# Kernel optimization log

Measured on AMD Instinct MI355X. Metric: run time of the kernel, lower is better.

The kernel has to match this reference:

```python
import jax, jax.numpy as jnp
import numpy as np

B, T, C, H = 2, 2048, 1024, 16
D = C // H  # head dim = 64

def setup_inputs() -> dict:
    key = jax.random.key(0)
    ks = jax.random.split(key, 5)
    s = 0.02
    return {
        "x": jax.random.normal(ks[0], (B, T, C), dtype=jnp.float32),
        "Wqkv": jax.random.normal(ks[1], (C, 3 * C), dtype=jnp.float32) * s,
        "bqkv": jnp.zeros((3 * C,), dtype=jnp.float32),
        "Wproj": jax.random.normal(ks[2], (C, C), dtype=jnp.float32) * s,
        "bproj": jnp.zeros((C,), dtype=jnp.float32),
    }

def reference(x, Wqkv, bqkv, Wproj, bproj):
    b, t, c = x.shape
    qkv = x @ Wqkv + bqkv                       # [B,T,3C]
    q, k, v = jnp.split(qkv, 3, axis=-1)
    # [B,T,C] -> [B,H,T,D]
    q = q.reshape(b, t, H, D).transpose(0, 2, 1, 3)
    k = k.reshape(b, t, H, D).transpose(0, 2, 1, 3)
    v = v.reshape(b, t, H, D).transpose(0, 2, 1, 3)
    scale = 1.0 / np.sqrt(D).astype(np.float32)
    attn = jnp.einsum('bhqd,bhkd->bhqk', q, k) * scale  # [B,H,T,T]
    causal = jnp.tril(jnp.ones((t, t), dtype=bool))
    attn = jnp.where(causal, attn, jnp.float32(-jnp.inf))
    attn = jax.nn.softmax(attn, axis=-1)
    y = jnp.einsum('bhqk,bhkd->bhqd', attn, v)          # [B,H,T,D]
    y = y.transpose(0, 2, 1, 3).reshape(b, t, c)        # [B,T,C]
    return y @ Wproj + bproj
```

## Files before the change

kernel.cpp:

```cpp
#include <hip/hip_runtime.h>
#include <stdint.h>

#define B_ 2
#define T_ 2048
#define C_ 1024
#define H_ 16
#define D_ 64
#define M_ (B_*T_)
#define BHTD_ (B_*H_*T_*D_)

typedef __bf16 bf16x8 __attribute__((ext_vector_type(8)));
typedef __bf16 bf16x4 __attribute__((ext_vector_type(4)));
typedef float f32x4 __attribute__((ext_vector_type(4)));

static __device__ __forceinline__ unsigned short f32_bf16(float f) {
    unsigned int u = __float_as_uint(f);
    u += 0x7FFFu + ((u >> 16) & 1u);
    return (unsigned short)(u >> 16);
}

__global__ void cast_kernel(const float* __restrict__ in, unsigned short* __restrict__ out, int n) {
    int i = (blockIdx.x * 256 + threadIdx.x) * 4;
    if (i >= n) return;
    float4 f = *(const float4*)(in + i);
    ushort4 o;
    o.x = f32_bf16(f.x); o.y = f32_bf16(f.y); o.z = f32_bf16(f.z); o.w = f32_bf16(f.w);
    *(ushort4*)(out + i) = o;
}

__global__ void transpose_cast_kernel(const float* __restrict__ W, unsigned short* __restrict__ Wt,
                                      int K, int N) {
    __shared__ float tile[32][33];
    int n0 = blockIdx.x * 32, k0 = blockIdx.y * 32;
    int tx = threadIdx.x, ty = threadIdx.y;
    #pragma unroll
    for (int j = 0; j < 32; j += 8)
        tile[ty + j][tx] = W[(size_t)(k0 + ty + j) * N + n0 + tx];
    __syncthreads();
    #pragma unroll
    for (int j = 0; j < 32; j += 8)
        Wt[(size_t)(n0 + ty + j) * K + k0 + tx] = f32_bf16(tile[tx][ty + j]);
}

template<int EPI>
__global__ __launch_bounds__(256) void gemm_bt(
    const unsigned short* __restrict__ A,
    const unsigned short* __restrict__ Bt,
    const float* __restrict__ bias,
    unsigned short* __restrict__ out_bf16,
    float* __restrict__ out_f32,
    int M, int N, int K)
{
    __shared__ unsigned short As[128 * 32];
    __shared__ unsigned short Bs[128 * 32];
    int tid = threadIdx.x;
    int lane = tid & 63, wid = tid >> 6;
    int fr = lane & 15, fg = lane >> 4;
    int row0 = blockIdx.x * 128, col0 = blockIdx.y * 128;
    int wm = (wid >> 1) * 64, wn = (wid & 1) * 64;

    f32x4 acc[4][4];
    #pragma unroll
    for (int i = 0; i < 4; ++i)
        #pragma unroll
        for (int j = 0; j < 4; ++j)
            acc[i][j] = (f32x4){0.f, 0.f, 0.f, 0.f};

    const int srw = lane >> 2;
    const int scl = (lane & 3) * 8;
    const int c0 = wid * 2, c1 = wid * 2 + 1;

    for (int k0 = 0; k0 < K; k0 += 32) {
        __syncthreads();
        __builtin_amdgcn_global_load_lds(
            (const __attribute__((address_space(1))) void*)(A + (size_t)(row0 + c0 * 16 + srw) * K + k0 + scl),
            (__attribute__((address_space(3))) void*)(As + c0 * 512), 16, 0, 0);
        __builtin_amdgcn_global_load_lds(
            (const __attribute__((address_space(1))) void*)(A + (size_t)(row0 + c1 * 16 + srw) * K + k0 + scl),
            (__attribute__((address_space(3))) void*)(As + c1 * 512), 16, 0, 0);
        __builtin_amdgcn_global_load_lds(
            (const __attribute__((address_space(1))) void*)(Bt + (size_t)(col0 + c0 * 16 + srw) * K + k0 + scl),
            (__attribute__((address_space(3))) void*)(Bs + c0 * 512), 16, 0, 0);
        __builtin_amdgcn_global_load_lds(
            (const __attribute__((address_space(1))) void*)(Bt + (size_t)(col0 + c1 * 16 + srw) * K + k0 + scl),
            (__attribute__((address_space(3))) void*)(Bs + c1 * 512), 16, 0, 0);
        __syncthreads();

        bf16x8 af[4], bfr[4];
        #pragma unroll
        for (int i = 0; i < 4; ++i) {
            af[i]  = *(const bf16x8*)(As + (wm + i * 16 + fr) * 32 + fg * 8);
            bfr[i] = *(const bf16x8*)(Bs + (wn + i * 16 + fr) * 32 + fg * 8);
        }
        #pragma unroll
        for (int mi = 0; mi < 4; ++mi)
            #pragma unroll
            for (int ni = 0; ni < 4; ++ni)
                acc[mi][ni] = __builtin_amdgcn_mfma_f32_16x16x32_bf16(af[mi], bfr[ni], acc[mi][ni], 0, 0, 0);
    }

    #pragma unroll
    for (int mi = 0; mi < 4; ++mi) {
        int rowb = row0 + wm + mi * 16 + fg * 4;
        #pragma unroll
        for (int ni = 0; ni < 4; ++ni) {
            int col = col0 + wn + ni * 16 + fr;
            float bv = bias[col];
            #pragma unroll
            for (int r = 0; r < 4; ++r) {
                float v = acc[mi][ni][r] + bv;
                int rr = rowb + r;
                if (EPI == 0) {
                    int part = col >> 10, c = col & 1023;
                    int h = c >> 6, d = c & 63;
                    int b = rr >> 11, t = rr & 2047;
                    if (part == 0) v *= 0.18033688011112042f;
                    size_t idx;
                    if (part == 2)
                        idx = (size_t)2 * BHTD_ + ((size_t)(b * H_ + h) * D_ + d) * T_ + t;
                    else
                        idx = (size_t)part * BHTD_ + ((size_t)(b * H_ + h) * T_ + t) * D_ + d;
                    out_bf16[idx] = f32_bf16(v);
                } else {
                    out_f32[(size_t)rr * N + col] = v;
                }
            }
        }
    }
}

__global__ __launch_bounds__(256) void attn_kernel(
    const unsigned short* __restrict__ qg,
    const unsigned short* __restrict__ kg,
    const unsigned short* __restrict__ vtg,
    unsigned short* __restrict__ y)
{
    const int id = blockIdx.x;
    const int xcd = id & 7, loc = id >> 3;
    const int bh = xcd * 4 + (loc & 3);
    const int iq = loc >> 2;
    const int chlo = iq, chhi = 31 - iq;
    const int b = bh >> 4, h = bh & 15;
    const int tid = threadIdx.x, wid = tid >> 6, lane = tid & 63;
    const int fr = lane & 15, fg = lane >> 4;

    const unsigned short* qp = qg + (size_t)bh * (T_ * D_);
    const unsigned short* kp = kg + (size_t)bh * (T_ * D_);
    const unsigned short* vp = vtg + (size_t)bh * (D_ * T_);

    __shared__ __align__(16) char Ks[2][64 * 128];
    __shared__ __align__(16) char Vs[2][64 * 128];
    __shared__ __align__(16) char Ps[4][32 * 128];
    char* Pw = Ps[wid];

    const int rhi = chhi * 64 + wid * 16;
    const int rlo = chlo * 64 + wid * 16;

    const int srow = tid >> 3;
    const int scb  = (tid & 7) * 16;
    const int sws  = scb ^ ((srow & 7) << 4);

    bf16x8 qhi[2], qlo[2];
    #pragma unroll
    for (int kd = 0; kd < 2; ++kd) {
        qhi[kd] = *(const bf16x8*)(qp + (size_t)(rhi + fr) * D_ + kd * 32 + fg * 8);
        qlo[kd] = *(const bf16x8*)(qp + (size_t)(rlo + fr) * D_ + kd * 32 + fg * 8);
    }

    f32x4 oHi[4], oLo[4];
    float lHi = 0.f, lLo = 0.f;
    #pragma unroll
    for (int n = 0; n < 4; ++n) {
        oHi[n] = (f32x4){0.f, 0.f, 0.f, 0.f};
        oLo[n] = (f32x4){0.f, 0.f, 0.f, 0.f};
    }

    const int ntk  = chhi + 1;
    const int ntlo = chlo + 1;

    {
        uint4 k0 = *(const uint4*)(kp + (size_t)srow        * D_ + (scb >> 1));
        uint4 k1 = *(const uint4*)(kp + (size_t)(srow + 32) * D_ + (scb >> 1));
        uint4 v0 = *(const uint4*)(vp + (size_t)srow        * T_ + (scb >> 1));
        uint4 v1 = *(const uint4*)(vp + (size_t)(srow + 32) * T_ + (scb >> 1));
        *(uint4*)(Ks[0] + srow * 128 + sws)        = k0;
        *(uint4*)(Ks[0] + (srow + 32) * 128 + sws) = k1;
        *(uint4*)(Vs[0] + srow * 128 + sws)        = v0;
        *(uint4*)(Vs[0] + (srow + 32) * 128 + sws) = v1;
    }
    __syncthreads();

    int cur = 0;
    for (int t = 0; t < ntk; ++t) {
        const int kv0 = t * 64;
        const int kv1 = (t + 1 < ntk) ? kv0 + 64 : kv0;

        uint4 pk0 = *(const uint4*)(kp + (size_t)(kv1 + srow)      * D_ + (scb >> 1));
        uint4 pk1 = *(const uint4*)(kp + (size_t)(kv1 + srow + 32) * D_ + (scb >> 1));
        uint4 pv0 = *(const uint4*)(vp + (size_t)srow        * T_ + kv1 + (scb >> 1));
        uint4 pv1 = *(const uint4*)(vp + (size_t)(srow + 32) * T_ + kv1 + (scb >> 1));

        const char* Kb = Ks[cur];
        const char* Vb = Vs[cur];
        const unsigned lsw = (unsigned)((fr & 7) << 4);
        const bool lo_act = (t < ntlo);

        f32x4 sh[4], sl[4];
        #pragma unroll
        for (int n = 0; n < 4; ++n) {
            sh[n] = (f32x4){0.f, 0.f, 0.f, 0.f};
            sl[n] = (f32x4){0.f, 0.f, 0.f, 0.f};
        }
        #pragma unroll
        for (int kd = 0; kd < 2; ++kd)
            #pragma unroll
            for (int n = 0; n < 4; ++n) {
                bf16x8 kf = *(const bf16x8*)(Kb + (n * 16 + fr) * 128 +
                                             (((unsigned)(kd * 64 + fg * 16)) ^ lsw));
                sh[n] = __builtin_amdgcn_mfma_f32_16x16x32_bf16(kf, qhi[kd], sh[n], 0, 0, 0);
                if (lo_act)
                    sl[n] = __builtin_amdgcn_mfma_f32_16x16x32_bf16(kf, qlo[kd], sl[n], 0, 0, 0);
            }

        {
            const bool masked = (t == chhi);
            const int qrow = rhi + fr;
            const unsigned prow = (unsigned)fr * 128;
            #pragma unroll
            for (int n = 0; n < 4; ++n) {
                float x0 = sh[n][0], x1 = sh[n][1], x2 = sh[n][2], x3 = sh[n][3];
                if (masked) {
                    const int kvb = kv0 + n * 16 + fg * 4;
                    if (kvb     > qrow) x0 = -1e30f;
                    if (kvb + 1 > qrow) x1 = -1e30f;
                    if (kvb + 2 > qrow) x2 = -1e30f;
                    if (kvb + 3 > qrow) x3 = -1e30f;
                }
                const float p0 = exp2f(x0), p1 = exp2f(x1);
                const float p2 = exp2f(x2), p3 = exp2f(x3);
                lHi += (p0 + p1) + (p2 + p3);
                bf16x4 pk4 = {(__bf16)p0, (__bf16)p1, (__bf16)p2, (__bf16)p3};
                *(uint2*)(Pw + ((prow + (unsigned)(n * 32 + fg * 8)) ^ lsw)) =
                    __builtin_bit_cast(uint2, pk4);
            }
        }
        if (lo_act) {
            const bool masked = (t == chlo);
            const int qrow = rlo + fr;
            const unsigned prow = (unsigned)(16 + fr) * 128;
            #pragma unroll
            for (int n = 0; n < 4; ++n) {
                float x0 = sl[n][0], x1 = sl[n][1], x2 = sl[n][2], x3 = sl[n][3];
                if (masked) {
                    const int kvb = kv0 + n * 16 + fg * 4;
                    if (kvb     > qrow) x0 = -1e30f;
                    if (kvb + 1 > qrow) x1 = -1e30f;
                    if (kvb + 2 > qrow) x2 = -1e30f;
                    if (kvb + 3 > qrow) x3 = -1e30f;
                }
                const float p0 = exp2f(x0), p1 = exp2f(x1);
                const float p2 = exp2f(x2), p3 = exp2f(x3);
                lLo += (p0 + p1) + (p2 + p3);
                bf16x4 pk4 = {(__bf16)p0, (__bf16)p1, (__bf16)p2, (__bf16)p3};
                *(uint2*)(Pw + ((prow + (unsigned)(n * 32 + fg * 8)) ^ lsw)) =
                    __builtin_bit_cast(uint2, pk4);
            }
        }
        asm volatile("s_waitcnt lgkmcnt(0)" ::: "memory");
        __builtin_amdgcn_sched_barrier(0);

        bf16x8 vf[4][2];
        #pragma unroll
        for (int nd = 0; nd < 4; ++nd)
            #pragma unroll
            for (int kk = 0; kk < 2; ++kk)
                vf[nd][kk] = *(const bf16x8*)(Vb + (nd * 16 + fr) * 128 +
                                              (((unsigned)(kk * 64 + fg * 16)) ^ lsw));
        {
            const unsigned prow = (unsigned)fr * 128;
            #pragma unroll
            for (int kk = 0; kk < 2; ++kk) {
                bf16x8 pb = *(const bf16x8*)(Pw + ((prow + (unsigned)(kk * 64 + fg * 16)) ^ lsw));
                #pragma unroll
                for (int nd = 0; nd < 4; ++nd)
                    oHi[nd] = __builtin_amdgcn_mfma_f32_16x16x32_bf16(vf[nd][kk], pb, oHi[nd], 0, 0, 0);
            }
        }
        if (lo_act) {
            const unsigned prow = (unsigned)(16 + fr) * 128;
            #pragma unroll
            for (int kk = 0; kk < 2; ++kk) {
                bf16x8 pb = *(const bf16x8*)(Pw + ((prow + (unsigned)(kk * 64 + fg * 16)) ^ lsw));
                #pragma unroll
                for (int nd = 0; nd < 4; ++nd)
                    oLo[nd] = __builtin_amdgcn_mfma_f32_16x16x32_bf16(vf[nd][kk], pb, oLo[nd], 0, 0, 0);
            }
        }

        {
            char* Kn = Ks[cur ^ 1];
            char* Vn = Vs[cur ^ 1];
            *(uint4*)(Kn + srow * 128 + sws)        = pk0;
            *(uint4*)(Kn + (srow + 32) * 128 + sws) = pk1;
            *(uint4*)(Vn + srow * 128 + sws)        = pv0;
            *(uint4*)(Vn + (srow + 32) * 128 + sws) = pv1;
        }
        __syncthreads();
        cur ^= 1;
    }

    #pragma unroll
    for (int s = 0; s < 2; ++s) {
        float rs = s ? lLo : lHi;
        rs += __shfl_xor(rs, 16);
        rs += __shfl_xor(rs, 32);
        const float inv = 1.f / rs;
        const int trow = (s ? rlo : rhi) + fr;
        f32x4* oT = s ? oLo : oHi;
        #pragma unroll
        for (int nd = 0; nd < 4; ++nd) {
            bf16x4 ov = {(__bf16)(oT[nd][0] * inv), (__bf16)(oT[nd][1] * inv),
                         (__bf16)(oT[nd][2] * inv), (__bf16)(oT[nd][3] * inv)};
            *(uint2*)(y + ((size_t)b * T_ + trow) * C_ + h * 64 + nd * 16 + fg * 4) =
                __builtin_bit_cast(uint2, ov);
        }
    }
}

extern "C" void kernel_launch(void* const* d_in, const int* in_sizes, int n_in,
                              void* d_out, int out_size, void* d_ws, size_t ws_size,
                              hipStream_t stream) {
    const float* x     = (const float*)d_in[0];
    const float* Wqkv  = (const float*)d_in[1];
    const float* bqkv  = (const float*)d_in[2];
    const float* Wproj = (const float*)d_in[3];
    const float* bproj = (const float*)d_in[4];
    float* out = (float*)d_out;

    char* ws = (char*)d_ws;
    unsigned short* x_bf    = (unsigned short*)(ws);
    unsigned short* wqkv_t  = (unsigned short*)(ws + 8388608);
    unsigned short* wproj_t = (unsigned short*)(ws + 14680064);
    unsigned short* qkv     = (unsigned short*)(ws + 16777216);
    unsigned short* ybuf    = (unsigned short*)(ws + 41943040);

    cast_kernel<<<(M_ * C_) / 4 / 256, 256, 0, stream>>>(x, x_bf, M_ * C_);
    transpose_cast_kernel<<<dim3(3072 / 32, 1024 / 32), dim3(32, 8), 0, stream>>>(Wqkv, wqkv_t, 1024, 3072);
    transpose_cast_kernel<<<dim3(1024 / 32, 1024 / 32), dim3(32, 8), 0, stream>>>(Wproj, wproj_t, 1024, 1024);

    gemm_bt<0><<<dim3(M_ / 128, 3072 / 128), 256, 0, stream>>>(
        x_bf, wqkv_t, bqkv, qkv, nullptr, M_, 3072, 1024);

    attn_kernel<<<dim3(512), 256, 0, stream>>>(
        qkv, qkv + (size_t)BHTD_, qkv + 2 * (size_t)BHTD_, ybuf);

    gemm_bt<1><<<dim3(M_ / 128, 1024 / 128), 256, 0, stream>>>(
        ybuf, wproj_t, bproj, nullptr, out, M_, 1024, 1024);
}
```

Measured before the change: 133.7 us.

## Double-buffer GEMM LDS tiles and interleave attention PV MMAs with softmax

The GEMM now keeps two LDS buffers for the A and B tiles and issues the global-to-LDS loads for the next k-step before computing the current one, with one barrier per iteration instead of two. This is meant to overlap global memory latency with MFMA work. The attention kernel loads the V fragments earlier and runs the hi-row PV MMAs right after writing the hi P tile, before the lo-row softmax, and it drops the explicit lgkmcnt wait and sched_barrier. The aim is to overlap exp computation with matrix work. The risk is ordering: the P tile is read back by other lanes without an explicit wait or barrier, and the async LDS loads may not be waited on correctly before they are read.

```diff
diff --git a/kernel.cpp b/kernel.cpp
--- a/kernel.cpp
+++ b/kernel.cpp
@@ -51,8 +51,8 @@
     float* __restrict__ out_f32,
     int M, int N, int K)
 {
-    __shared__ unsigned short As[128 * 32];
-    __shared__ unsigned short Bs[128 * 32];
+    __shared__ unsigned short As[2][128 * 32];
+    __shared__ unsigned short Bs[2][128 * 32];
     int tid = threadIdx.x;
     int lane = tid & 63, wid = tid >> 6;
     int fr = lane & 15, fg = lane >> 4;
@@ -70,33 +70,42 @@
     const int scl = (lane & 3) * 8;
     const int c0 = wid * 2, c1 = wid * 2 + 1;
 
-    for (int k0 = 0; k0 < K; k0 += 32) {
-        __syncthreads();
+    auto stage = [&](int buf, int k0) {
         __builtin_amdgcn_global_load_lds(
             (const __attribute__((address_space(1))) void*)(A + (size_t)(row0 + c0 * 16 + srw) * K + k0 + scl),
-            (__attribute__((address_space(3))) void*)(As + c0 * 512), 16, 0, 0);
+            (__attribute__((address_space(3))) void*)(As[buf] + c0 * 512), 16, 0, 0);
         __builtin_amdgcn_global_load_lds(
             (const __attribute__((address_space(1))) void*)(A + (size_t)(row0 + c1 * 16 + srw) * K + k0 + scl),
-            (__attribute__((address_space(3))) void*)(As + c1 * 512), 16, 0, 0);
+            (__attribute__((address_space(3))) void*)(As[buf] + c1 * 512), 16, 0, 0);
         __builtin_amdgcn_global_load_lds(
             (const __attribute__((address_space(1))) void*)(Bt + (size_t)(col0 + c0 * 16 + srw) * K + k0 + scl),
-            (__attribute__((address_space(3))) void*)(Bs + c0 * 512), 16, 0, 0);
+            (__attribute__((address_space(3))) void*)(Bs[buf] + c0 * 512), 16, 0, 0);
         __builtin_amdgcn_global_load_lds(
             (const __attribute__((address_space(1))) void*)(Bt + (size_t)(col0 + c1 * 16 + srw) * K + k0 + scl),
-            (__attribute__((address_space(3))) void*)(Bs + c1 * 512), 16, 0, 0);
-        __syncthreads();
+            (__attribute__((address_space(3))) void*)(Bs[buf] + c1 * 512), 16, 0, 0);
+    };
+
+    stage(0, 0);
+    __syncthreads();
+
+    int cur = 0;
+    for (int k0 = 0; k0 < K; k0 += 32) {
+        if (k0 + 32 < K) stage(cur ^ 1, k0 + 32);
 
         bf16x8 af[4], bfr[4];
         #pragma unroll
         for (int i = 0; i < 4; ++i) {
-            af[i]  = *(const bf16x8*)(As + (wm + i * 16 + fr) * 32 + fg * 8);
-            bfr[i] = *(const bf16x8*)(Bs + (wn + i * 16 + fr) * 32 + fg * 8);
+            af[i]  = *(const bf16x8*)(As[cur] + (wm + i * 16 + fr) * 32 + fg * 8);
+            bfr[i] = *(const bf16x8*)(Bs[cur] + (wn + i * 16 + fr) * 32 + fg * 8);
         }
         #pragma unroll
         for (int mi = 0; mi < 4; ++mi)
             #pragma unroll
             for (int ni = 0; ni < 4; ++ni)
                 acc[mi][ni] = __builtin_amdgcn_mfma_f32_16x16x32_bf16(af[mi], bfr[ni], acc[mi][ni], 0, 0, 0);
+
+        __syncthreads();
+        cur ^= 1;
     }
 
     #pragma unroll
@@ -222,6 +231,14 @@
                     sl[n] = __builtin_amdgcn_mfma_f32_16x16x32_bf16(kf, qlo[kd], sl[n], 0, 0, 0);
             }
 
+        bf16x8 vf[4][2];
+        #pragma unroll
+        for (int nd = 0; nd < 4; ++nd)
+            #pragma unroll
+            for (int kk = 0; kk < 2; ++kk)
+                vf[nd][kk] = *(const bf16x8*)(Vb + (nd * 16 + fr) * 128 +
+                                              (((unsigned)(kk * 64 + fg * 16)) ^ lsw));
+
         {
             const bool masked = (t == chhi);
             const int qrow = rhi + fr;
@@ -244,6 +261,16 @@
                     __builtin_bit_cast(uint2, pk4);
             }
         }
+        {
+            const unsigned prow = (unsigned)fr * 128;
+            #pragma unroll
+            for (int kk = 0; kk < 2; ++kk) {
+                bf16x8 pb = *(const bf16x8*)(Pw + ((prow + (unsigned)(kk * 64 + fg * 16)) ^ lsw));
+                #pragma unroll
+                for (int nd = 0; nd < 4; ++nd)
+                    oHi[nd] = __builtin_amdgcn_mfma_f32_16x16x32_bf16(vf[nd][kk], pb, oHi[nd], 0, 0, 0);
+            }
+        }
         if (lo_act) {
             const bool masked = (t == chlo);
             const int qrow = rlo + fr;
@@ -265,32 +292,10 @@
                 *(uint2*)(Pw + ((prow + (unsigned)(n * 32 + fg * 8)) ^ lsw)) =
                     __builtin_bit_cast(uint2, pk4);
             }
-        }
-        asm volatile("s_waitcnt lgkmcnt(0)" ::: "memory");
-        __builtin_amdgcn_sched_barrier(0);
-
-        bf16x8 vf[4][2];
-        #pragma unroll
-        for (int nd = 0; nd < 4; ++nd)
-            #pragma unroll
-            for (int kk = 0; kk < 2; ++kk)
-                vf[nd][kk] = *(const bf16x8*)(Vb + (nd * 16 + fr) * 128 +
-                                              (((unsigned)(kk * 64 + fg * 16)) ^ lsw));
-        {
-            const unsigned prow = (unsigned)fr * 128;
+            const unsigned prow2 = (unsigned)(16 + fr) * 128;
             #pragma unroll
             for (int kk = 0; kk < 2; ++kk) {
-                bf16x8 pb = *(const bf16x8*)(Pw + ((prow + (unsigned)(kk * 64 + fg * 16)) ^ lsw));
-                #pragma unroll
-                for (int nd = 0; nd < 4; ++nd)
-                    oHi[nd] = __builtin_amdgcn_mfma_f32_16x16x32_bf16(vf[nd][kk], pb, oHi[nd], 0, 0, 0);
-            }
-        }
-        if (lo_act) {
-            const unsigned prow = (unsigned)(16 + fr) * 128;
-            #pragma unroll
-            for (int kk = 0; kk < 2; ++kk) {
-                bf16x8 pb = *(const bf16x8*)(Pw + ((prow + (unsigned)(kk * 64 + fg * 16)) ^ lsw));
+                bf16x8 pb = *(const bf16x8*)(Pw + ((prow2 + (unsigned)(kk * 64 + fg * 16)) ^ lsw));
                 #pragma unroll
                 for (int nd = 0; nd < 4; ++nd)
                     oLo[nd] = __builtin_amdgcn_mfma_f32_16x16x32_bf16(vf[nd][kk], pb, oLo[nd], 0, 0, 0);
```

New measurement: 126.5 us. -5.3%, faster.
